# Performance work log

Hardware: AMD Instinct MI355X
Metric: run time of the kernel (lower is better)

The kernel has to match this reference:

```python
import jax, jax.numpy as jnp
import numpy as np

H, C = 5, 128          # heads, hidden_channels
NUM_GRAPHS = 500
N_NODES, N_EDGES = 20000, 320000


def gat_layer(x, edge_attr, src, dst, W, We, a_src, a_dst, a_edge, b):
    """PyG GATConv with edge_dim, add_self_loops=True, fill_value='mean', concat heads."""
    N = x.shape[0]
    ed = edge_attr.dtype
    # self-loop edge_attr = scatter-mean of incoming edge_attr per target node
    deg = jax.ops.segment_sum(jnp.ones((dst.shape[0],), ed), dst, num_segments=N)
    loop_attr = jax.ops.segment_sum(edge_attr, dst, num_segments=N) / jnp.maximum(deg, 1.0)[:, None]
    loop = jnp.arange(N, dtype=src.dtype)
    s = jnp.concatenate([src, loop])
    d = jnp.concatenate([dst, loop])
    ea = jnp.concatenate([edge_attr, loop_attr], axis=0)
    h = (x @ W).reshape(N, H, C)            # [N,H,C]
    e = (ea @ We).reshape(-1, H, C)         # [E2,H,C]
    a_l = (h * a_src).sum(-1)               # [N,H]
    a_r = (h * a_dst).sum(-1)               # [N,H]
    a_e = (e * a_edge).sum(-1)              # [E2,H]
    alpha = jax.nn.leaky_relu(a_l[s] + a_r[d] + a_e, 0.2)
    # segment softmax over destination neighborhoods
    amax = jax.ops.segment_max(alpha, d, num_segments=N)
    ex = jnp.exp(alpha - amax[d])
    denom = jax.ops.segment_sum(ex, d, num_segments=N)
    att = ex / (denom[d] + 1e-16)           # [E2,H]
    msg = h[s] * att[..., None]             # [E2,H,C]
    out = jax.ops.segment_sum(msg, d, num_segments=N).reshape(N, H * C)
    return out + b


def setup_inputs() -> dict:
    key = jax.random.key(0)
    ks = jax.random.split(key, 24)
    p = lambda k, sh: (jax.random.normal(k, sh, dtype=jnp.float32) * 0.05)
    inp = {
        "x": jax.random.normal(ks[0], (N_NODES, 43), dtype=jnp.float32),
        "edge_attr": jax.random.normal(ks[1], (N_EDGES, 10), dtype=jnp.float32),
        "W1": p(ks[2], (43, H * C)),   "We1": p(ks[3], (10, H * C)),
        "asrc1": p(ks[4], (H, C)), "adst1": p(ks[5], (H, C)), "aedge1": p(ks[6], (H, C)),
        "b1": jnp.zeros((H * C,), jnp.float32),
        "W2": p(ks[7], (H * C, H * C)), "We2": p(ks[8], (10, H * C)),
        "asrc2": p(ks[9], (H, C)), "adst2": p(ks[10], (H, C)), "aedge2": p(ks[11], (H, C)),
        "b2": jnp.zeros((H * C,), jnp.float32),
        "W3": p(ks[12], (H * C, H * C)), "We3": p(ks[13], (10, H * C)),
        "asrc3": p(ks[14], (H, C)), "adst3": p(ks[15], (H, C)), "aedge3": p(ks[16], (H, C)),
        "b3": jnp.zeros((H * C,), jnp.float32),
        "Wlin": p(ks[17], (H * C, 1)), "blin": jnp.zeros((1,), jnp.float32),
        "edge_index": jax.random.randint(ks[18], (2, N_EDGES), 0, N_NODES, dtype=jnp.int32),
        "batch": jnp.sort(jax.random.randint(ks[19], (N_NODES,), 0, NUM_GRAPHS, dtype=jnp.int32)),
    }
    return inp


def reference(x, edge_attr, W1, We1, asrc1, adst1, aedge1, b1,
              W2, We2, asrc2, adst2, aedge2, b2,
              W3, We3, asrc3, adst3, aedge3, b3,
              Wlin, blin, edge_index, batch):
    src, dst = edge_index[0], edge_index[1]
    h = jax.nn.relu(gat_layer(x, edge_attr, src, dst, W1, We1, asrc1, adst1, aedge1, b1))
    h = jax.nn.relu(gat_layer(h, edge_attr, src, dst, W2, We2, asrc2, adst2, aedge2, b2))
    h = gat_layer(h, edge_attr, src, dst, W3, We3, asrc3, adst3, aedge3, b3)
    # global mean pool over graphs
    cnt = jax.ops.segment_sum(jnp.ones((h.shape[0],), h.dtype), batch, num_segments=NUM_GRAPHS)
    pooled = jax.ops.segment_sum(h, batch, num_segments=NUM_GRAPHS) / jnp.maximum(cnt, 1.0)[:, None]
    return (pooled @ Wlin + blin).squeeze(-1)   # [NUM_GRAPHS]
```

## Files before the change

kernel.cpp:

```cpp
#include <hip/hip_runtime.h>

#define N_NODESC 20000
#define N_EDGESC 320000
#define HC 640
#define NGRAPH 500

typedef unsigned short u16;
typedef unsigned int u32;
typedef __attribute__((ext_vector_type(8))) short bf16x8;
typedef __attribute__((ext_vector_type(4))) float f32x4;

__device__ __forceinline__ float wred_sum(float v){
  #pragma unroll
  for(int o=32;o;o>>=1) v += __shfl_xor(v,o,64);
  return v;
}
__device__ __forceinline__ float lrelu(float x){ return x>0.f? x:0.2f*x; }

__device__ __forceinline__ u16 f2bf(float f){
  u32 u=__float_as_uint(f);
  u32 r=u+0x7FFFu+((u>>16)&1u);
  return (u16)(r>>16);
}
__device__ __forceinline__ float bf2f(u16 s){ return __uint_as_float(((u32)s)<<16); }
__device__ __forceinline__ float bflo(u32 w){ return __uint_as_float(w<<16); }
__device__ __forceinline__ float bfhi(u32 w){ return __uint_as_float(w&0xFFFF0000u); }

__device__ __forceinline__ void gload16(const void* g, void* l){
  __builtin_amdgcn_global_load_lds((const __attribute__((address_space(1))) void*)g,
                                   (__attribute__((address_space(3))) void*)l, 16, 0, 0);
}

__device__ __forceinline__ size_t fidx(int r, int k, int KB){
  return ((size_t)(r>>4)*KB + (k>>5))*512 + (((k>>3)&3)*16 + (r&15))*8 + (k&7);
}


__global__ void k_count(const int* __restrict__ dst, int* __restrict__ cnt){
  int i=blockIdx.x*blockDim.x+threadIdx.x;
  if(i>=N_EDGESC) return;
  atomicAdd(&cnt[dst[i]],1);
}

__global__ void k_scan(const int* __restrict__ cnt, int* __restrict__ rptr, int* __restrict__ pos){
  __shared__ int ps[1024];
  int t=threadIdx.x;
  const int CH=20;
  int beg=t*CH, end=min(beg+CH, N_NODESC);
  int s=0;
  for(int i=beg;i<end;i++) s+=cnt[i];
  ps[t]=s; __syncthreads();
  for(int off=1;off<1024;off<<=1){
    int v=(t>=off)? ps[t-off]:0;
    __syncthreads();
    ps[t]+=v;
    __syncthreads();
  }
  int base=ps[t]-s;
  for(int i=beg;i<end;i++){ rptr[i]=base; pos[i]=base; base+=cnt[i]; }
}

__global__ void k_scatter(const int* __restrict__ dst, const int* __restrict__ src,
                          const float* __restrict__ eattr, int* __restrict__ pos,
                          int* __restrict__ srcE, int* __restrict__ dstC,
                          float* __restrict__ eattrC){
  int i=blockIdx.x*blockDim.x+threadIdx.x;
  if(i>=N_EDGESC) return;
  int d=dst[i];
  int j=atomicAdd(&pos[d],1);
  dstC[j]=d;
  srcE[j]=src[i];
  const float* ep=&eattr[(size_t)i*10];
  float* op=&eattrC[(size_t)j*10];
  #pragma unroll
  for(int k=0;k<10;k++) op[k]=ep[k];
}

__global__ __launch_bounds__(256) void k_loop_attr(const float* __restrict__ eattrC,
    const int* __restrict__ rptr, const int* __restrict__ cnt,
    float* __restrict__ lattr){
  int tid=threadIdx.x, lane=tid&63;
  int n=blockIdx.x*4+(tid>>6);
  if(n>=N_NODESC) return;
  int beg=rptr[n], deg=cnt[n];
  float s[10]={0,0,0,0,0,0,0,0,0,0};
  for(int off=lane; off<deg; off+=64){
    const float* ep=&eattrC[(size_t)(beg+off)*10];
    #pragma unroll
    for(int k=0;k<10;k++) s[k]+=ep[k];
  }
  float inv=1.f/fmaxf((float)deg,1.f);
  #pragma unroll
  for(int k=0;k<10;k++){
    float tot=wred_sum(s[k]);
    if(lane==0) lattr[(size_t)n*10+k]=tot*inv;
  }
}


__global__ void k_padxb(const float* __restrict__ x, u16* __restrict__ xb){
  int idx=blockIdx.x*blockDim.x+threadIdx.x;
  if(idx>=N_NODESC*64) return;
  int n=idx>>6, kk=idx&63;
  float v = kk<43 ? x[n*43+kk] : 0.f;
  xb[idx]=f2bf(v);
}

__global__ void k_conv_w3(const float* __restrict__ W0, const float* __restrict__ W1,
                          const float* __restrict__ W2,
                          u16* __restrict__ hi, u16* __restrict__ lo){
  const int R0=HC*64, R1=R0+HC*HC;
  const int TOT=R1+HC*HC;
  int idx=blockIdx.x*blockDim.x+threadIdx.x;
  if(idx>=TOT) return;
  const float* W; int local, KP, KL, base;
  if(idx<R0){ W=W0; local=idx; KP=64; KL=43; base=0; }
  else if(idx<R1){ W=W1; local=idx-R0; KP=HC; KL=HC; base=R0; }
  else { W=W2; local=idx-R1; KP=HC; KL=HC; base=R1; }
  int n=local/KP, kk=local-n*KP;
  float v = kk<KL ? W[(size_t)kk*HC+n] : 0.f;
  u16 h=f2bf(v);
  size_t off=(size_t)base + fidx(n,kk,KP>>5);
  hi[off]=h;
  lo[off]=f2bf(v-bf2f(h));
}


__global__ void k_ve3(const float* __restrict__ We0, const float* __restrict__ ae0,
                      const float* __restrict__ We1, const float* __restrict__ ae1,
                      const float* __restrict__ We2, const float* __restrict__ ae2,
                      float* __restrict__ ve3){
  int t=threadIdx.x;
  if(t>=150) return;
  int L=t/50, r=t-50*L, k=r/5, h=r%5;
  const float* We = (L==0)?We0:(L==1)?We1:We2;
  const float* ae = (L==0)?ae0:(L==1)?ae1:ae2;
  float s=0.f;
  for(int c=0;c<128;c++) s += We[k*HC + h*128 + c]*ae[h*128+c];
  ve3[t]=s;
}

__global__ void k_vs0(const float* __restrict__ W0, const float* __restrict__ asrc,
                      const float* __restrict__ adst,
                      const float* __restrict__ bias2, const float* __restrict__ wlin,
                      float* __restrict__ VS, float* __restrict__ VD,
                      float* __restrict__ cb){
  int t=threadIdx.x;
  if(t<320){
    int k=t/5, h=t%5;
    float sv=0.f, dv=0.f;
    if(k<43){
      for(int c=0;c<128;c++){
        float wv=W0[(size_t)k*HC + h*128 + c];
        sv+=wv*asrc[h*128+c];
        dv+=wv*adst[h*128+c];
      }
    }
    VS[t]=sv; VD[t]=dv;
  }else{
    int lane=t-320;
    float s=0.f;
    for(int c=lane;c<HC;c+=64) s+=bias2[c]*wlin[c];
    s=wred_sum(s);
    if(lane==0) cb[0]=s;
  }
}

__global__ __launch_bounds__(256) void k_alar0(const float* __restrict__ x,
    const float* __restrict__ VS, const float* __restrict__ VD,
    float* __restrict__ al, float* __restrict__ ar){
  __shared__ float vs[320], vd[320];
  if(threadIdx.x<320){ vs[threadIdx.x]=VS[threadIdx.x]; vd[threadIdx.x]=VD[threadIdx.x]; }
  __syncthreads();
  int idx=blockIdx.x*blockDim.x+threadIdx.x;
  if(idx>=N_NODESC*5) return;
  int n=idx/5, h=idx-5*n;
  float sa=0.f, sd=0.f;
  const float* xr=&x[(size_t)n*43];
  for(int k=0;k<43;k++){
    float xv=xr[k];
    sa+=xv*vs[k*5+h];
    sd+=xv*vd[k*5+h];
  }
  al[idx]=sa; ar[idx]=sd;
}

__global__ __launch_bounds__(256) void k_edge_terms3(const float* __restrict__ eattrC,
    const float* __restrict__ lattr, const float* __restrict__ ve3,
    float* __restrict__ aeC3, float* __restrict__ ael3){
  __shared__ float ves[150];
  if(threadIdx.x<150) ves[threadIdx.x]=ve3[threadIdx.x];
  __syncthreads();
  const int NEDGET=N_EDGESC+N_NODESC*5;
  int idx=blockIdx.x*blockDim.x+threadIdx.x;
  if(idx>=3*NEDGET) return;
  int L=idx/NEDGET, r=idx-L*NEDGET;
  const float* vl=&ves[L*50];
  if(r<N_EDGESC){
    float ev[10];
    const float* ep=&eattrC[(size_t)r*10];
    #pragma unroll
    for(int k=0;k<10;k++) ev[k]=ep[k];
    #pragma unroll
    for(int hh=0;hh<5;hh++){
      float s=0.f;
      #pragma unroll
      for(int k=0;k<10;k++) s+=ev[k]*vl[k*5+hh];
      aeC3[(size_t)L*N_EDGESC*5 + (size_t)r*5+hh]=s;
    }
  }else{
    int t=r-N_EDGESC;
    int n=t/5, h=t-5*n;
    float s=0.f;
    #pragma unroll
    for(int k=0;k<10;k++) s+=lattr[(size_t)n*10+k]*vl[k*5+h];
    ael3[(size_t)L*N_NODESC*5 + t]=s;
  }
}

__global__ void k_edgew(const int* __restrict__ srcE, const int* __restrict__ dstC,
                        const float* __restrict__ al, const float* __restrict__ ar,
                        const float* __restrict__ aeC, float* __restrict__ wE){
  int j=blockIdx.x*blockDim.x+threadIdx.x;
  if(j>=N_EDGESC) return;
  int s=srcE[j], d=dstC[j];
  const float* av=&aeC[(size_t)j*5];
  float* wp=&wE[(size_t)j*5];
  #pragma unroll
  for(int h=0;h<5;h++)
    wp[h]=__expf(lrelu(al[s*5+h]+ar[d*5+h]+av[h]));
}


__global__ __launch_bounds__(256) void k_aggx(const u16* __restrict__ xb,
    const int* __restrict__ srcE, const int* __restrict__ rptr, const int* __restrict__ cnt,
    const float* __restrict__ al, const float* __restrict__ ar, const float* __restrict__ ael,
    const float* __restrict__ wE,
    u16* __restrict__ aggx, float* __restrict__ den0){
  const size_t HSZ=(size_t)N_NODESC*64;
  int tid=threadIdx.x, lane=tid&63;
  int n=blockIdx.x*4+(tid>>6);
  if(n>=N_NODESC) return;
  float den[5], acc[5];
  #pragma unroll
  for(int h=0;h<5;h++)
    den[h]=__expf(lrelu(al[n*5+h]+ar[n*5+h]+ael[n*5+h]));
  float xn=bf2f(xb[(size_t)n*64+lane]);
  #pragma unroll
  for(int h=0;h<5;h++) acc[h]=den[h]*xn;
  int beg=rptr[n], end=beg+cnt[n];
  int j=beg;
  for(; j+7<end; j+=8){
    int sj[8]; float xv[8];
    #pragma unroll
    for(int u=0;u<8;u++) sj[u]=srcE[j+u];
    #pragma unroll
    for(int u=0;u<8;u++) xv[u]=bf2f(xb[(size_t)sj[u]*64+lane]);
    #pragma unroll
    for(int u=0;u<8;u++){
      const float* wp=&wE[(size_t)(j+u)*5];
      #pragma unroll
      for(int h=0;h<5;h++){
        float w=wp[h];
        den[h]+=w;
        acc[h]+=w*xv[u];
      }
    }
  }
  for(; j<end; j++){
    int sj=srcE[j];
    float xv=bf2f(xb[(size_t)sj*64+lane]);
    const float* wp=&wE[(size_t)j*5];
    #pragma unroll
    for(int h=0;h<5;h++){
      float w=wp[h];
      den[h]+=w;
      acc[h]+=w*xv;
    }
  }
  size_t fo=fidx(n,lane,2);
  #pragma unroll
  for(int h=0;h<5;h++) aggx[(size_t)h*HSZ+fo]=f2bf(acc[h]);
  if(lane<5) den0[(size_t)n*5+lane]=den[lane];
}

__global__ __launch_bounds__(256,3) void k_gemm_l0b(
    const u16* __restrict__ AGX,
    const u16* __restrict__ Bhi, const u16* __restrict__ Blo,
    const float* __restrict__ den0, const float* __restrict__ bias,
    u16* __restrict__ A1, int M, int nblk){
  const size_t HSZ=(size_t)N_NODESC*64;
  __shared__ u16 lds[2*3*4096];
  int tid=threadIdx.x;
  int lane=tid&63;
  int w=tid>>6;
  int l15=lane&15, lg=lane>>4;
  int orig=blockIdx.x;
  int q=nblk>>3, r=nblk&7;
  int xcd=orig&7, off=orig>>3;
  int wg=(xcd<r? xcd*(q+1) : r*(q+1)+(xcd-r)*q)+off;
  int by=wg/5, bx=wg-5*by;
  int row0=by*128, col0=bx*128;
  int wr=w>>1, wc=w&1;
  const u16* A=AGX+(size_t)bx*HSZ;

  f32x4 zero = {0.f,0.f,0.f,0.f};
  f32x4 acc[4][4];
  #pragma unroll
  for(int i=0;i<4;i++)
    #pragma unroll
    for(int j=0;j<4;j++) acc[i][j]=zero;

  auto stage=[&](int b, int k0){
    u16* base = lds + b*3*4096;
    int kb=k0>>5;
    #pragma unroll
    for(int c=0;c<2;c++){
      int sb=w+4*c;
      size_t af=((size_t)((row0>>4)+sb)*2 + kb)*512 + lane*8;
      size_t bf=((size_t)((col0>>4)+sb)*2 + kb)*512 + lane*8;
      gload16(A+af, base + sb*512);
      gload16(Bhi+bf, base+4096 + sb*512);
      gload16(Blo+bf, base+8192 + sb*512);
    }
  };

  stage(0,0);
  __syncthreads();
  int cur=0;
  for(int t=0;t<2;t++){
    if(t==0) stage(1,32);
    u16* cb = lds + cur*3*4096;
    bf16x8 ah[4], bh[4], bl[4];
    #pragma unroll
    for(int i=0;i<4;i++){
      ah[i]=*(const bf16x8*)&cb[(wr*4+i)*512 + lane*8];
      bh[i]=*(const bf16x8*)&cb[4096+(wc*4+i)*512 + lane*8];
      bl[i]=*(const bf16x8*)&cb[8192+(wc*4+i)*512 + lane*8];
    }
    #pragma unroll
    for(int i=0;i<4;i++)
      #pragma unroll
      for(int j=0;j<4;j++){
        acc[i][j]=__builtin_amdgcn_mfma_f32_16x16x32_bf16(ah[i],bh[j],acc[i][j],0,0,0);
        acc[i][j]=__builtin_amdgcn_mfma_f32_16x16x32_bf16(ah[i],bl[j],acc[i][j],0,0,0);
      }
    __syncthreads();
    cur^=1;
  }

  #pragma unroll
  for(int i=0;i<4;i++){
    #pragma unroll
    for(int j=0;j<4;j++){
      int col=col0+wc*64+j*16+l15;
      float bv=bias[col];
      #pragma unroll
      for(int rr=0;rr<4;rr++){
        int row=row0+wr*64+i*16+lg*4+rr;
        if(row<M){
          float dv=den0[(size_t)row*5+bx];
          float v=acc[i][j][rr]/(dv+1e-16f)+bv;
          v=fmaxf(v,0.f);
          A1[fidx(row,col,20)]=f2bf(v);
        }
      }
    }
  }
}


template<bool HB, bool QOUT>
__global__ __launch_bounds__(256,3) void k_gemm64(
    const u16* __restrict__ A,
    const u16* __restrict__ B,
    const float* __restrict__ asrc, const float* __restrict__ adst,
    const float* __restrict__ wlin,
    u16* __restrict__ hb, float* __restrict__ al, float* __restrict__ ar,
    float* __restrict__ qn,
    int M, int KP, int nblk){
  __shared__ u16 lds[4*6144];
  int tid=threadIdx.x;
  int lane=tid&63;
  int w=tid>>6;
  int l15=lane&15, lg=lane>>4;
  int orig=blockIdx.x;
  int q=nblk>>3, r=nblk&7;
  int xcd=orig&7, off=orig>>3;
  int wg=(xcd<r? xcd*(q+1) : r*(q+1)+(xcd-r)*q)+off;
  int by=wg/5, bx=wg-5*by;
  int row0=by*64, col0=bx*128;
  int KB=KP>>5;

  f32x4 zero = {0.f,0.f,0.f,0.f};
  f32x4 acc[4][2];
  #pragma unroll
  for(int i=0;i<4;i++){ acc[i][0]=zero; acc[i][1]=zero; }

  auto stage=[&](int b, int k0){
    u16* base = lds + b*6144;
    int kb=k0>>5;
    size_t af=((size_t)((row0>>4)+w)*KB + kb)*512 + lane*8;
    gload16(A+af, base + w*512);
    #pragma unroll
    for(int c=0;c<2;c++){
      int sb=w+4*c;
      size_t bf=((size_t)((col0>>4)+sb)*KB + kb)*512 + lane*8;
      gload16(B+bf, base+2048 + sb*512);
    }
  };

  int nt=KP/32;
  stage(0,0);
  stage(1,32);
  for(int t=0;t<nt;t++){
    int nb=t+2;
    if(nb<nt) stage(nb&3, nb*32);
    if(nb<nt)      { asm volatile("s_waitcnt vmcnt(6)" ::: "memory"); }
    else if(t+1<nt){ asm volatile("s_waitcnt vmcnt(3)" ::: "memory"); }
    else           { asm volatile("s_waitcnt vmcnt(0)" ::: "memory"); }
    __builtin_amdgcn_sched_barrier(0);
    __builtin_amdgcn_s_barrier();
    u16* cb = lds + (t&3)*6144;
    bf16x8 ah[4], bh[2];
    #pragma unroll
    for(int i=0;i<4;i++) ah[i]=*(const bf16x8*)&cb[i*512 + lane*8];
    #pragma unroll
    for(int j=0;j<2;j++) bh[j]=*(const bf16x8*)&cb[2048+(w*2+j)*512 + lane*8];
    #pragma unroll
    for(int i=0;i<4;i++){
      acc[i][0]=__builtin_amdgcn_mfma_f32_16x16x32_bf16(ah[i],bh[0],acc[i][0],0,0,0);
      acc[i][1]=__builtin_amdgcn_mfma_f32_16x16x32_bf16(ah[i],bh[1],acc[i][1],0,0,0);
    }
  }
  __syncthreads();

  float asv[2], adv[2], wlv[2];
  #pragma unroll
  for(int j=0;j<2;j++){
    int c=col0+w*32+j*16+l15;
    asv[j]=asrc[c]; adv[j]=adst[c];
    if(QOUT) wlv[j]=wlin[c];
  }
  if(HB){
    #pragma unroll
    for(int i=0;i<4;i++){
      #pragma unroll
      for(int j=0;j<2;j++){
        #pragma unroll
        for(int rr=0;rr<4;rr++){
          int row=row0+i*16+lg*4+rr;
          if(row<M)
            hb[(size_t)row*HC + ((w&1)*32+j*16+l15)*10 + bx*2+(w>>1)]=f2bf(acc[i][j][rr]);
        }
      }
    }
  }
  float* redAl=(float*)lds;
  float* redAr=redAl+256;
  float* redQ =redAr+256;
  #pragma unroll
  for(int i=0;i<4;i++){
    #pragma unroll
    for(int rr=0;rr<4;rr++){
      float sa=0.f, sd=0.f, sq=0.f;
      #pragma unroll
      for(int j=0;j<2;j++){
        sa+=acc[i][j][rr]*asv[j];
        sd+=acc[i][j][rr]*adv[j];
        if(QOUT) sq+=acc[i][j][rr]*wlv[j];
      }
      #pragma unroll
      for(int o=1;o<16;o<<=1){
        sa+=__shfl_xor(sa,o,64); sd+=__shfl_xor(sd,o,64);
        if(QOUT) sq+=__shfl_xor(sq,o,64);
      }
      if(l15==0){
        int lr=i*16+lg*4+rr;
        redAl[lr*4+w]=sa; redAr[lr*4+w]=sd;
        if(QOUT) redQ[lr*4+w]=sq;
      }
    }
  }
  __syncthreads();
  if(tid<64){
    int row=row0+tid;
    if(row<M){
      al[(size_t)row*5+bx]=redAl[tid*4]+redAl[tid*4+1]+redAl[tid*4+2]+redAl[tid*4+3];
      ar[(size_t)row*5+bx]=redAr[tid*4]+redAr[tid*4+1]+redAr[tid*4+2]+redAr[tid*4+3];
      if(QOUT) qn[(size_t)row*5+bx]=redQ[tid*4]+redQ[tid*4+1]+redQ[tid*4+2]+redQ[tid*4+3];
    }
  }
}

__global__ __launch_bounds__(256) void k_agg(const u16* __restrict__ hb, const int* __restrict__ srcE,
    const int* __restrict__ rptr, const int* __restrict__ cnt,
    const float* __restrict__ al, const float* __restrict__ ar, const float* __restrict__ ael,
    const float* __restrict__ wE, const float* __restrict__ bias,
    u16* __restrict__ ohi){
  int tid=threadIdx.x, lane=tid&63;
  int n=blockIdx.x*4+(tid>>6);
  if(n>=N_NODESC) return;
  float den[5], acc[10];
  #pragma unroll
  for(int h=0;h<5;h++)
    den[h]=__expf(lrelu(al[n*5+h]+ar[n*5+h]+ael[n*5+h]));
  {
    const u32* sp=(const u32*)(hb+(size_t)n*HC+lane*10);
    #pragma unroll
    for(int j2=0;j2<5;j2++){
      u32 wv=sp[j2];
      acc[2*j2]  =den[j2]*bflo(wv);
      acc[2*j2+1]=den[j2]*bfhi(wv);
    }
  }
  int beg=rptr[n], end=beg+cnt[n];
  int j=beg;
  for(; j+3<end; j+=4){
    int sj[4];
    #pragma unroll
    for(int u=0;u<4;u++) sj[u]=srcE[j+u];
    float w[4][5];
    #pragma unroll
    for(int u=0;u<4;u++){
      const float* wp=&wE[(size_t)(j+u)*5];
      #pragma unroll
      for(int h=0;h<5;h++) w[u][h]=wp[h];
    }
    u32 wv[4][5];
    #pragma unroll
    for(int u=0;u<4;u++){
      const u32* hr=(const u32*)(hb+(size_t)sj[u]*HC+lane*10);
      #pragma unroll
      for(int j2=0;j2<5;j2++) wv[u][j2]=hr[j2];
    }
    #pragma unroll
    for(int u=0;u<4;u++){
      #pragma unroll
      for(int j2=0;j2<5;j2++){
        den[j2]+=w[u][j2];
        acc[2*j2]  +=w[u][j2]*bflo(wv[u][j2]);
        acc[2*j2+1]+=w[u][j2]*bfhi(wv[u][j2]);
      }
    }
  }
  for(; j<end; j++){
    int sj=srcE[j];
    const float* wp=&wE[(size_t)j*5];
    float w[5];
    #pragma unroll
    for(int h=0;h<5;h++){ w[h]=wp[h]; den[h]+=w[h]; }
    const u32* hr=(const u32*)(hb+(size_t)sj*HC+lane*10);
    #pragma unroll
    for(int j2=0;j2<5;j2++){
      u32 wv=hr[j2];
      acc[2*j2]  +=w[j2]*bflo(wv);
      acc[2*j2+1]+=w[j2]*bfhi(wv);
    }
  }
  #pragma unroll
  for(int k=0;k<10;k++){
    int ccol=lane+64*k;
    float vv=acc[k]/(den[k>>1]+1e-16f)+bias[ccol];
    vv=fmaxf(vv,0.f);
    ohi[fidx(n,ccol,20)]=f2bf(vv);
  }
}

__global__ __launch_bounds__(256) void k_agg_last(const float* __restrict__ qn,
    const int* __restrict__ srcE, const int* __restrict__ rptr, const int* __restrict__ cnt,
    const float* __restrict__ al, const float* __restrict__ ar, const float* __restrict__ ael,
    const float* __restrict__ aeC, const float* __restrict__ cb,
    float* __restrict__ pnode){
  int tid=threadIdx.x;
  int sub=tid&15;
  int n=blockIdx.x*16+(tid>>4);
  if(n>=N_NODESC) return;
  float arn[5], den[5], qs[5];
  #pragma unroll
  for(int h=0;h<5;h++) arn[h]=ar[n*5+h];
  #pragma unroll
  for(int h=0;h<5;h++){ den[h]=0.f; qs[h]=0.f; }
  if(sub==0){
    #pragma unroll
    for(int h=0;h<5;h++){
      float pp=__expf(lrelu(al[n*5+h]+arn[h]+ael[n*5+h]));
      den[h]=pp; qs[h]=pp*qn[(size_t)n*5+h];
    }
  }
  int beg=rptr[n], deg=cnt[n];
  for(int off=sub; off<deg; off+=16){
    int j=beg+off;
    int s=srcE[j];
    const float* av=&aeC[(size_t)j*5];
    const float* qv=&qn[(size_t)s*5];
    #pragma unroll
    for(int h=0;h<5;h++){
      float pp=__expf(lrelu(al[s*5+h]+arn[h]+av[h]));
      den[h]+=pp; qs[h]+=pp*qv[h];
    }
  }
  #pragma unroll
  for(int h=0;h<5;h++){
    #pragma unroll
    for(int o=1;o<16;o<<=1){
      den[h]+=__shfl_xor(den[h],o,16);
      qs[h]+=__shfl_xor(qs[h],o,16);
    }
  }
  if(sub==0){
    float s=0.f;
    #pragma unroll
    for(int h=0;h<5;h++) s+=qs[h]/(den[h]+1e-16f);
    pnode[n]=s+cb[0];
  }
}

__global__ __launch_bounds__(256) void k_graphout(const float* __restrict__ pnode,
    const int* __restrict__ batch, const float* __restrict__ blin,
    float* __restrict__ out){
  int tid=threadIdx.x, lane=tid&63;
  int g=blockIdx.x*4+(tid>>6);
  if(g>=NGRAPH) return;
  auto lb=[&](int val){
    int lo=0, hi=N_NODESC;
    while(lo<hi){ int mid=(lo+hi)>>1; if(batch[mid]<val) lo=mid+1; else hi=mid; }
    return lo;
  };
  int s0=lb(g), s1=lb(g+1);
  float s=0.f;
  for(int i=s0+lane;i<s1;i+=64) s+=pnode[i];
  s=wred_sum(s);
  if(lane==0) out[g]=s/fmaxf((float)(s1-s0),1.f)+blin[0];
}


extern "C" void kernel_launch(void* const* d_in, const int* in_sizes, int n_in,
                              void* d_out, int out_size, void* d_ws, size_t ws_size,
                              hipStream_t stream){
  const float* x     = (const float*)d_in[0];
  const float* eattr = (const float*)d_in[1];
  const float* W[3]    ={(const float*)d_in[2],(const float*)d_in[8],(const float*)d_in[14]};
  const float* We[3]   ={(const float*)d_in[3],(const float*)d_in[9],(const float*)d_in[15]};
  const float* asrc[3] ={(const float*)d_in[4],(const float*)d_in[10],(const float*)d_in[16]};
  const float* adst[3] ={(const float*)d_in[5],(const float*)d_in[11],(const float*)d_in[17]};
  const float* aedge[3]={(const float*)d_in[6],(const float*)d_in[12],(const float*)d_in[18]};
  const float* bias[3] ={(const float*)d_in[7],(const float*)d_in[13],(const float*)d_in[19]};
  const float* Wlin  = (const float*)d_in[20];
  const float* blin  = (const float*)d_in[21];
  const int* eind    = (const int*)d_in[22];
  const int* srcp    = eind;
  const int* dstp    = eind + N_EDGESC;
  const int* batch   = (const int*)d_in[23];
  float* out = (float*)d_out;

  char* ws=(char*)d_ws;
  size_t o=0;
  auto alloc=[&](size_t bytes)->void*{ void* p=ws+o; o=(o+bytes+255)&~(size_t)255; return p; };
  u16* hb   =(u16*)alloc((size_t)N_NODESC*HC*2);
  u16* Ahi =(u16*)alloc((size_t)N_NODESC*HC*2);
  u16* xb  =(u16*)alloc((size_t)N_NODESC*64*2);
  u16* aggx=(u16*)alloc((size_t)5*N_NODESC*64*2);
  const int WB0=0, WB1=HC*64, WB2=WB1+HC*HC;
  u16* Bthi3=(u16*)alloc((size_t)(WB2+HC*HC)*2);
  u16* Btlo3=(u16*)alloc((size_t)(WB2+HC*HC)*2);
  float* al   =(float*)alloc((size_t)N_NODESC*5*4);
  float* ar   =(float*)alloc((size_t)N_NODESC*5*4);
  float* qn   =(float*)alloc((size_t)N_NODESC*5*4);
  float* den0 =(float*)alloc((size_t)N_NODESC*5*4);
  float* ael3 =(float*)alloc((size_t)3*N_NODESC*5*4);
  float* aeC3 =(float*)alloc((size_t)3*N_EDGESC*5*4);
  float* wE   =(float*)alloc((size_t)N_EDGESC*5*4);
  float* lattr=(float*)alloc((size_t)N_NODESC*10*4);
  float* eattrC=(float*)alloc((size_t)N_EDGESC*10*4);
  float* ve3  =(float*)alloc(256*4);
  float* VS0  =(float*)alloc(320*4);
  float* VD0  =(float*)alloc(320*4);
  float* cbv  =(float*)alloc(64*4);
  float* pnode=(float*)alloc((size_t)N_NODESC*4);
  int* cntI   =(int*)alloc((size_t)N_NODESC*4);
  int* rptr   =(int*)alloc((size_t)N_NODESC*4);
  int* pos    =(int*)alloc((size_t)N_NODESC*4);
  int* srcE   =(int*)alloc((size_t)N_EDGESC*4);
  int* dstC   =(int*)alloc((size_t)N_EDGESC*4);

  hipMemsetAsync(cntI,0,(size_t)N_NODESC*4,stream);

  k_count<<<(N_EDGESC+255)/256,256,0,stream>>>(dstp,cntI);
  k_scan<<<1,1024,0,stream>>>(cntI,rptr,pos);
  k_scatter<<<(N_EDGESC+255)/256,256,0,stream>>>(dstp,srcp,eattr,pos,srcE,dstC,eattrC);
  k_loop_attr<<<(N_NODESC+3)/4,256,0,stream>>>(eattrC,rptr,cntI,lattr);
  k_padxb<<<(N_NODESC*64+255)/256,256,0,stream>>>(x,xb);
  k_ve3<<<1,256,0,stream>>>(We[0],aedge[0],We[1],aedge[1],We[2],aedge[2],ve3);
  k_vs0<<<1,384,0,stream>>>(W[0],asrc[0],adst[0],bias[2],Wlin,VS0,VD0,cbv);
  {
    int tot=WB2+HC*HC;
    k_conv_w3<<<(tot+255)/256,256,0,stream>>>(W[0],W[1],W[2],Bthi3,Btlo3);
  }
  {
    const int NEDGET=N_EDGESC+N_NODESC*5;
    k_edge_terms3<<<(3*NEDGET+255)/256,256,0,stream>>>(eattrC,lattr,ve3,aeC3,ael3);
  }
  k_alar0<<<(N_NODESC*5+255)/256,256,0,stream>>>(x,VS0,VD0,al,ar);

  const int NBLK0=5*((N_NODESC+127)/128);
  const int NBLK64=5*((N_NODESC+63)/64);

  k_edgew<<<(N_EDGESC+255)/256,256,0,stream>>>(srcE,dstC,al,ar,aeC3,wE);
  k_aggx<<<(N_NODESC+3)/4,256,0,stream>>>(xb,srcE,rptr,cntI,al,ar,ael3,wE,aggx,den0);
  k_gemm_l0b<<<NBLK0,256,0,stream>>>(aggx,Bthi3+WB0,Btlo3+WB0,den0,bias[0],Ahi,N_NODESC,NBLK0);

  {
    const float* aeL = aeC3 + (size_t)1*N_EDGESC*5;
    const float* aelL= ael3 + (size_t)1*N_NODESC*5;
    k_gemm64<true,false><<<NBLK64,256,0,stream>>>(Ahi,Bthi3+WB1,
        asrc[1],adst[1],Wlin,hb,al,ar,qn,N_NODESC,HC,NBLK64);
    k_edgew<<<(N_EDGESC+255)/256,256,0,stream>>>(srcE,dstC,al,ar,aeL,wE);
    k_agg<<<(N_NODESC+3)/4,256,0,stream>>>(hb,srcE,rptr,cntI,al,ar,aelL,wE,bias[1],Ahi);
  }
  {
    const float* aelL= ael3 + (size_t)2*N_NODESC*5;
    k_gemm64<false,true><<<NBLK64,256,0,stream>>>(Ahi,Bthi3+WB2,
        asrc[2],adst[2],Wlin,hb,al,ar,qn,N_NODESC,HC,NBLK64);
    k_agg_last<<<(N_NODESC+15)/16,256,0,stream>>>(qn,srcE,rptr,cntI,al,ar,aelL,aeC3+(size_t)2*N_EDGESC*5,cbv,pnode);
  }
  k_graphout<<<(NGRAPH+3)/4,256,0,stream>>>(pnode,batch,blin,out);
}
```

Before: 379.2 us.

## Fold layer-3 weights into 15 projection vectors, replacing the full GEMM

For the last layer only three per-head projections of h are needed (attention source, attention destination, and the pooled linear output). The weight matrix is therefore pre-multiplied with asrc, adst and wlin into a 640x15 matrix. A small matvec-style kernel over the bf16 activations then replaces the 640x640 GEMM that produced those projections. This removes most of the layer-3 FLOPs, at the cost of FP32 scalar FMAs, a one-off precompute kernel and a different rounding order.

```diff
diff --git a/kernel.cpp b/kernel.cpp
--- a/kernel.cpp
+++ b/kernel.cpp
@@ -164,6 +164,21 @@
     s=wred_sum(s);
     if(lane==0) cb[0]=s;
   }
+}
+
+__global__ void k_vq2(const float* __restrict__ W2, const float* __restrict__ asrc,
+                      const float* __restrict__ adst, const float* __restrict__ wlin,
+                      float* __restrict__ V2){
+  int t=blockIdx.x*blockDim.x+threadIdx.x;
+  if(t>=HC*15) return;
+  int k=t/15, o=t-15*k;
+  int h=o%5, grp=o/5;
+  const float* v = (grp==0)? asrc : (grp==1)? adst : wlin;
+  const float* wr=&W2[(size_t)k*HC + h*128];
+  const float* vr=&v[h*128];
+  float s=0.f;
+  for(int c=0;c<128;c++) s+=wr[c]*vr[c];
+  V2[t]=s;
 }
 
 __global__ __launch_bounds__(256) void k_alar0(const float* __restrict__ x,
@@ -370,14 +385,11 @@
 }
 
 
-template<bool HB, bool QOUT>
 __global__ __launch_bounds__(256,3) void k_gemm64(
     const u16* __restrict__ A,
     const u16* __restrict__ B,
     const float* __restrict__ asrc, const float* __restrict__ adst,
-    const float* __restrict__ wlin,
     u16* __restrict__ hb, float* __restrict__ al, float* __restrict__ ar,
-    float* __restrict__ qn,
     int M, int KP, int nblk){
   __shared__ u16 lds[4*6144];
   int tid=threadIdx.x;
@@ -435,50 +447,43 @@
   }
   __syncthreads();
 
-  float asv[2], adv[2], wlv[2];
+  float asv[2], adv[2];
   #pragma unroll
   for(int j=0;j<2;j++){
     int c=col0+w*32+j*16+l15;
     asv[j]=asrc[c]; adv[j]=adst[c];
-    if(QOUT) wlv[j]=wlin[c];
-  }
-  if(HB){
-    #pragma unroll
-    for(int i=0;i<4;i++){
-      #pragma unroll
-      for(int j=0;j<2;j++){
-        #pragma unroll
-        for(int rr=0;rr<4;rr++){
-          int row=row0+i*16+lg*4+rr;
-          if(row<M)
-            hb[(size_t)row*HC + ((w&1)*32+j*16+l15)*10 + bx*2+(w>>1)]=f2bf(acc[i][j][rr]);
-        }
+  }
+  #pragma unroll
+  for(int i=0;i<4;i++){
+    #pragma unroll
+    for(int j=0;j<2;j++){
+      #pragma unroll
+      for(int rr=0;rr<4;rr++){
+        int row=row0+i*16+lg*4+rr;
+        if(row<M)
+          hb[(size_t)row*HC + ((w&1)*32+j*16+l15)*10 + bx*2+(w>>1)]=f2bf(acc[i][j][rr]);
       }
     }
   }
   float* redAl=(float*)lds;
   float* redAr=redAl+256;
-  float* redQ =redAr+256;
   #pragma unroll
   for(int i=0;i<4;i++){
     #pragma unroll
     for(int rr=0;rr<4;rr++){
-      float sa=0.f, sd=0.f, sq=0.f;
+      float sa=0.f, sd=0.f;
       #pragma unroll
       for(int j=0;j<2;j++){
         sa+=acc[i][j][rr]*asv[j];
         sd+=acc[i][j][rr]*adv[j];
-        if(QOUT) sq+=acc[i][j][rr]*wlv[j];
       }
       #pragma unroll
       for(int o=1;o<16;o<<=1){
         sa+=__shfl_xor(sa,o,64); sd+=__shfl_xor(sd,o,64);
-        if(QOUT) sq+=__shfl_xor(sq,o,64);
       }
       if(l15==0){
         int lr=i*16+lg*4+rr;
         redAl[lr*4+w]=sa; redAr[lr*4+w]=sd;
-        if(QOUT) redQ[lr*4+w]=sq;
       }
     }
   }
@@ -488,8 +493,51 @@
     if(row<M){
       al[(size_t)row*5+bx]=redAl[tid*4]+redAl[tid*4+1]+redAl[tid*4+2]+redAl[tid*4+3];
       ar[(size_t)row*5+bx]=redAr[tid*4]+redAr[tid*4+1]+redAr[tid*4+2]+redAr[tid*4+3];
-      if(QOUT) qn[(size_t)row*5+bx]=redQ[tid*4]+redQ[tid*4+1]+redQ[tid*4+2]+redQ[tid*4+3];
-    }
+    }
+  }
+}
+
+__global__ __launch_bounds__(256) void k_qal2(const u16* __restrict__ A2,
+    const float* __restrict__ V2,
+    float* __restrict__ al, float* __restrict__ ar, float* __restrict__ qn){
+  __shared__ float Vs[HC*15];
+  __shared__ float red[4][16][15];
+  int tid=threadIdx.x, lane=tid&63, w=tid>>6;
+  for(int i=tid;i<HC*15;i+=256) Vs[i]=V2[i];
+  __syncthreads();
+  int nb=blockIdx.x;
+  int koct=lane>>4;
+  float acc[15];
+  #pragma unroll
+  for(int o=0;o<15;o++) acc[o]=0.f;
+  for(int kb=w*5; kb<w*5+5; kb++){
+    bf16x8 v=*(const bf16x8*)&A2[((size_t)nb*20+kb)*512 + (size_t)lane*8];
+    #pragma unroll
+    for(int e=0;e<8;e++){
+      float xv=bf2f((u16)v[e]);
+      int k=kb*32+koct*8+e;
+      const float* vp=&Vs[k*15];
+      #pragma unroll
+      for(int o=0;o<15;o++) acc[o]+=xv*vp[o];
+    }
+  }
+  #pragma unroll
+  for(int o=0;o<15;o++){
+    acc[o]+=__shfl_xor(acc[o],16,64);
+    acc[o]+=__shfl_xor(acc[o],32,64);
+  }
+  if((lane&15)==lane){
+    #pragma unroll
+    for(int o=0;o<15;o++) red[w][lane][o]=acc[o];
+  }
+  __syncthreads();
+  if(tid<240){
+    int node=tid/15, o=tid-15*node;
+    float s=red[0][node][o]+red[1][node][o]+red[2][node][o]+red[3][node][o];
+    int n=nb*16+node;
+    if(o<5)       al[(size_t)n*5+o]=s;
+    else if(o<10) ar[(size_t)n*5+(o-5)]=s;
+    else          qn[(size_t)n*5+(o-10)]=s;
   }
 }
 
@@ -676,6 +724,7 @@
   float* ve3  =(float*)alloc(256*4);
   float* VS0  =(float*)alloc(320*4);
   float* VD0  =(float*)alloc(320*4);
+  float* V2   =(float*)alloc((size_t)HC*15*4);
   float* cbv  =(float*)alloc(64*4);
   float* pnode=(float*)alloc((size_t)N_NODESC*4);
   int* cntI   =(int*)alloc((size_t)N_NODESC*4);
@@ -693,6 +742,7 @@
   k_padxb<<<(N_NODESC*64+255)/256,256,0,stream>>>(x,xb);
   k_ve3<<<1,256,0,stream>>>(We[0],aedge[0],We[1],aedge[1],We[2],aedge[2],ve3);
   k_vs0<<<1,384,0,stream>>>(W[0],asrc[0],adst[0],bias[2],Wlin,VS0,VD0,cbv);
+  k_vq2<<<(HC*15+255)/256,256,0,stream>>>(W[2],asrc[2],adst[2],Wlin,V2);
   {
     int tot=WB2+HC*HC;
     k_conv_w3<<<(tot+255)/256,256,0,stream>>>(W[0],W[1],W[2],Bthi3,Btlo3);
@@ -713,15 +763,14 @@
   {
     const float* aeL = aeC3 + (size_t)1*N_EDGESC*5;
     const float* aelL= ael3 + (size_t)1*N_NODESC*5;
-    k_gemm64<true,false><<<NBLK64,256,0,stream>>>(Ahi,Bthi3+WB1,
-        asrc[1],adst[1],Wlin,hb,al,ar,qn,N_NODESC,HC,NBLK64);
+    k_gemm64<<<NBLK64,256,0,stream>>>(Ahi,Bthi3+WB1,
+        asrc[1],adst[1],hb,al,ar,N_NODESC,HC,NBLK64);
     k_edgew<<<(N_EDGESC+255)/256,256,0,stream>>>(srcE,dstC,al,ar,aeL,wE);
     k_agg<<<(N_NODESC+3)/4,256,0,stream>>>(hb,srcE,rptr,cntI,al,ar,aelL,wE,bias[1],Ahi);
   }
   {
     const float* aelL= ael3 + (size_t)2*N_NODESC*5;
-    k_gemm64<false,true><<<NBLK64,256,0,stream>>>(Ahi,Bthi3+WB2,
-        asrc[2],adst[2],Wlin,hb,al,ar,qn,N_NODESC,HC,NBLK64);
+    k_qal2<<<N_NODESC/16,256,0,stream>>>(Ahi,V2,al,ar,qn);
     k_agg_last<<<(N_NODESC+15)/16,256,0,stream>>>(qn,srcE,rptr,cntI,al,ar,aelL,aeC3+(size_t)2*N_EDGESC*5,cbv,pnode);
   }
   k_graphout<<<(NGRAPH+3)/4,256,0,stream>>>(pnode,batch,blin,out);
```

Result: no change. 371.9 us (-1.9%).
